# Performance work log

Measured on AMD Instinct MI355X. Metric: run time of the kernel, lower is better.

## Reference

```python
import jax, jax.numpy as jnp
import numpy as np

N = 100000      # nodes
E = 1600000     # edges (before self-loops)
IN = 128        # in_dim
HID = 128       # hidden_dim
H = 4           # heads
D = HID // H    # head_dim = 32
L = 3           # n_layers
G = 128         # graphs in batch
NEG_SLOPE = 0.2 # PyG GATConv default leaky_relu slope
BN_EPS = 1e-5


def setup_inputs() -> dict:
    key = jax.random.key(0)
    ks = jax.random.split(key, 16)
    x = jax.random.normal(ks[0], (N, IN), dtype=jnp.float32)
    edge_index = jax.random.randint(ks[1], (2, E), 0, N, dtype=jnp.int64)
    batch = jnp.sort(jax.random.randint(ks[2], (N,), 0, G, dtype=jnp.int64))
    # stacked per-layer GATConv params (in_dim == hidden_dim so all layers stack)
    W = jax.random.normal(ks[3], (L, HID, HID), dtype=jnp.float32) * (1.0 / np.sqrt(HID))
    att_src = jax.random.normal(ks[4], (L, H, D), dtype=jnp.float32) * 0.1
    att_dst = jax.random.normal(ks[5], (L, H, D), dtype=jnp.float32) * 0.1
    bias = jax.random.normal(ks[6], (L, HID), dtype=jnp.float32) * 0.01
    # BatchNorm1d (eval mode: running stats)
    gamma = 1.0 + 0.1 * jax.random.normal(ks[7], (L, HID), dtype=jnp.float32)
    beta = 0.01 * jax.random.normal(ks[8], (L, HID), dtype=jnp.float32)
    bn_mean = jnp.zeros((L, HID), dtype=jnp.float32)
    bn_var = jnp.ones((L, HID), dtype=jnp.float32)
    # MLP head: Linear(HID, HID//2) -> ReLU -> Linear(HID//2, 1)
    Wh1 = jax.random.normal(ks[9], (HID, HID // 2), dtype=jnp.float32) * (1.0 / np.sqrt(HID))
    bh1 = jnp.zeros((HID // 2,), dtype=jnp.float32)
    Wh2 = jax.random.normal(ks[10], (HID // 2, 1), dtype=jnp.float32) * (1.0 / np.sqrt(HID // 2))
    bh2 = jnp.zeros((1,), dtype=jnp.float32)
    return {"x": x, "edge_index": edge_index, "batch": batch, "W": W,
            "att_src": att_src, "att_dst": att_dst, "bias": bias,
            "gamma": gamma, "beta": beta, "bn_mean": bn_mean, "bn_var": bn_var,
            "Wh1": Wh1, "bh1": bh1, "Wh2": Wh2, "bh2": bh2}


def _gat_conv(x, src, dst, W_l, asrc, adst, b):
    # x: [N, F_in]; src/dst: [E+N] (self-loops included); returns [N, H*D]
    h = (x @ W_l).reshape(N, H, D)                      # [N,H,D]
    a_s = jnp.einsum('nhd,hd->nh', h, asrc)             # [N,H]
    a_d = jnp.einsum('nhd,hd->nh', h, adst)
    e = jax.nn.leaky_relu(a_s[src] + a_d[dst], NEG_SLOPE)  # [Etot,H]
    # segment softmax over incoming edges per destination node
    e_max = jax.ops.segment_max(e, dst, num_segments=N)    # [N,H]
    p = jnp.exp(e - e_max[dst])
    denom = jax.ops.segment_sum(p, dst, num_segments=N)    # [N,H]
    alpha = p / (denom[dst] + 1e-16)                        # [Etot,H]
    msg = h[src] * alpha[:, :, None]                        # [Etot,H,D]
    out = jax.ops.segment_sum(msg, dst, num_segments=N)     # [N,H,D]
    return out.reshape(N, H * D) + b


def reference(x, edge_index, batch, W, att_src, att_dst, bias,
              gamma, beta, bn_mean, bn_var, Wh1, bh1, Wh2, bh2):
    # add self-loops once (PyG GATConv default add_self_loops=True)
    loop = jnp.arange(N, dtype=edge_index.dtype)
    src = jnp.concatenate([edge_index[0], loop])
    dst = jnp.concatenate([edge_index[1], loop])
    for l in range(L):
        x = _gat_conv(x, src, dst, W[l], att_src[l], att_dst[l], bias[l])
        x = jnp.maximum(x, 0.0)
        # BatchNorm1d, eval mode (dropout is identity in eval)
        x = (x - bn_mean[l]) * (gamma[l] / jnp.sqrt(bn_var[l] + BN_EPS)) + beta[l]
    # global mean pool over graphs
    sums = jax.ops.segment_sum(x, batch, num_segments=G)            # [G,HID]
    cnts = jax.ops.segment_sum(jnp.ones((N,), x.dtype), batch, num_segments=G)
    pooled = sums / jnp.maximum(cnts, 1.0)[:, None]
    hdn = jnp.maximum(pooled @ Wh1 + bh1, 0.0)
    return (hdn @ Wh2 + bh2).squeeze(-1)                            # [G]
```

## Files before the change

kernel.cpp:

```cpp
#include <hip/hip_runtime.h>
#include <hip/hip_fp16.h>


typedef __bf16 bf16x8 __attribute__((ext_vector_type(8)));
typedef float  f32x4  __attribute__((ext_vector_type(4)));
typedef unsigned int u32x4 __attribute__((ext_vector_type(4)));

#define BCOLS 144
#define BSTRIDE (BCOLS * 128)

#define MAXBKT 800
#define BCAP   4096

__global__ __launch_bounds__(256)
void k_bucket(const int* __restrict__ ei, unsigned int* __restrict__ bkt,
              int* __restrict__ bcnt, int Ne, int Nn, int nbkt) {
    __shared__ int lcnt[MAXBKT];
    __shared__ int lbase[MAXBKT];
    int tid = threadIdx.x;
    for (int i = tid; i < nbkt; i += 256) lcnt[i] = 0;
    __syncthreads();
    int chunk0 = blockIdx.x * 8192;
    int nnz = Ne + Nn;
    for (int i = 0; i < 32; ++i) {
        int e = chunk0 + i * 256 + tid;
        if (e < nnz) {
            int d = (e < Ne) ? ei[Ne + e] : (e - Ne);
            atomicAdd(&lcnt[d >> 7], 1);
        }
    }
    __syncthreads();
    for (int b = tid; b < nbkt; b += 256) {
        int c = lcnt[b];
        lbase[b] = (c > 0) ? atomicAdd(&bcnt[b], c) : 0;
        lcnt[b] = 0;
    }
    __syncthreads();
    for (int i = 0; i < 32; ++i) {
        int e = chunk0 + i * 256 + tid;
        if (e < nnz) {
            int s, d;
            if (e < Ne) { s = ei[e]; d = ei[Ne + e]; }
            else        { s = e - Ne; d = e - Ne; }
            int b = d >> 7;
            int r = atomicAdd(&lcnt[b], 1);
            bkt[(long)b * BCAP + lbase[b] + r] = ((unsigned)s << 7) | (unsigned)(d & 127);
        }
    }
}

__global__ __launch_bounds__(256)
void k_bhist(const unsigned int* __restrict__ bkt, const int* __restrict__ bcnt,
             int* __restrict__ deg, int Nn) {
    __shared__ int h[128];
    int b = blockIdx.x;
    int tid = threadIdx.x;
    if (tid < 128) h[tid] = 0;
    __syncthreads();
    int cnt = bcnt[b];
    const unsigned int* bp = bkt + (long)b * BCAP;
    for (int i = tid; i < cnt; i += 256)
        atomicAdd(&h[bp[i] & 127], 1);
    __syncthreads();
    int node = b * 128 + tid;
    if (tid < 128 && node < Nn) deg[node] = h[tid];
}

__global__ __launch_bounds__(256)
void k_bscatter(const unsigned int* __restrict__ bkt, const int* __restrict__ bcnt,
                const int* __restrict__ rowptr, int* __restrict__ colv, int Nn) {
    __shared__ int cur[128];
    int b = blockIdx.x;
    int tid = threadIdx.x;
    int node = b * 128 + tid;
    if (tid < 128) cur[tid] = (node < Nn) ? rowptr[node] : 0;
    __syncthreads();
    int cnt = bcnt[b];
    const unsigned int* bp = bkt + (long)b * BCAP;
    for (int i = tid; i < cnt; i += 256) {
        unsigned int e = bp[i];
        int pos = atomicAdd(&cur[e & 127], 1);
        colv[pos] = (int)(e >> 7);
    }
}

__global__ __launch_bounds__(512)
void k_scan_partial(int* __restrict__ deg, int* __restrict__ tmp,
                    int* __restrict__ bsum, int Nn) {
    __shared__ int s0[512], s1[512];
    int t = threadIdx.x;
    int gi = blockIdx.x * 512 + t;
    int v = (gi < Nn) ? deg[gi] : 0;
    s0[t] = v;
    __syncthreads();
    int* src = s0; int* dst = s1;
    for (int off = 1; off < 512; off <<= 1) {
        int x = src[t];
        if (t >= off) x += src[t - off];
        dst[t] = x;
        __syncthreads();
        int* tw = src; src = dst; dst = tw;
    }
    if (gi < Nn) tmp[gi] = src[t];
    if (t == 511) bsum[blockIdx.x] = src[511];
}

__global__ __launch_bounds__(256)
void k_scan_bsums(int* bsum, int nb) {
    __shared__ int s0[256], s1[256];
    int t = threadIdx.x;
    int v = (t < nb) ? bsum[t] : 0;
    s0[t] = v;
    __syncthreads();
    int* src = s0; int* dst = s1;
    for (int off = 1; off < 256; off <<= 1) {
        int x = src[t];
        if (t >= off) x += src[t - off];
        dst[t] = x;
        __syncthreads();
        int* tw = src; src = dst; dst = tw;
    }
    if (t < nb) bsum[t] = src[t] - v;
}

__global__ void k_scan_add(const int* __restrict__ tmp, const int* __restrict__ bsum,
                           int* __restrict__ rowptr, int Nn) {
    int gi = blockIdx.x * 256 + threadIdx.x;
    if (gi < Nn) rowptr[gi + 1] = tmp[gi] + bsum[gi >> 9];
    if (gi == 0) rowptr[0] = 0;
}

__global__ void k_prep(const float* __restrict__ gamma, const float* __restrict__ beta,
                       const float* __restrict__ mean, const float* __restrict__ var,
                       float* __restrict__ bn_mul, float* __restrict__ bn_add,
                       const float* __restrict__ W, const float* __restrict__ asrc,
                       const float* __restrict__ adst,
                       __bf16* __restrict__ Hi, __bf16* __restrict__ Lo) {
    int gid = blockIdx.x * 256 + threadIdx.x;
    if (gid < 384) {
        float sc = gamma[gid] / sqrtf(var[gid] + 1e-5f);
        bn_mul[gid] = sc;
        bn_add[gid] = beta[gid] - mean[gid] * sc;
    }
    if (gid < 3 * 128 * 128) {
        int l = gid >> 14;
        int k = (gid >> 7) & 127;
        int n = gid & 127;
        float f = W[gid];
        __bf16 h = (__bf16)f;
        int o = l * BSTRIDE + n * 128 + k;
        Hi[o] = h;
        Lo[o] = (__bf16)(f - (float)h);
    }
    if (gid < 3 * 128 * 8) {
        int l = gid >> 10;
        int r = gid & 1023;
        int k = r >> 3;
        int j = r & 7;
        int hh = j & 3;
        const float* av = (j < 4 ? asrc : adst) + l * 128 + hh * 32;
        const float* wp = W + l * 16384 + k * 128 + hh * 32;
        float sum = 0.f;
#pragma unroll
        for (int d = 0; d < 32; ++d) sum = fmaf(wp[d], av[d], sum);
        __bf16 h = (__bf16)sum;
        int o = l * BSTRIDE + (128 + j) * 128 + k;
        Hi[o] = h;
        Lo[o] = (__bf16)(sum - (float)h);
    }
    if (gid < 3 * 128 * 8) {
        int l = gid >> 10;
        int r = gid & 1023;
        int k = r >> 3;
        int j = r & 7;
        int o = l * BSTRIDE + (136 + j) * 128 + k;
        Hi[o] = (__bf16)0.f;
        Lo[o] = (__bf16)0.f;
    }
}

__global__ __launch_bounds__(256)
void k_gemm_mfma(const float* __restrict__ X, const __bf16* __restrict__ BtHi,
                 const __bf16* __restrict__ BtLo, __half* __restrict__ Hout,
                 float* __restrict__ as_, float* __restrict__ ad_, int Nn) {
    int t = threadIdx.x;
    int w = t >> 6;
    int lane = t & 63;
    int li = lane & 15;
    int b  = lane >> 4;
    long rowBase = (long)blockIdx.x * 128 + w * 32;

    float4 xf[2][4][2];
#pragma unroll
    for (int rt = 0; rt < 2; ++rt) {
        long r = rowBase + rt * 16 + li;
        if (r > Nn - 1) r = Nn - 1;
        const float4* xp = (const float4*)(X + r * 128);
#pragma unroll
        for (int ks = 0; ks < 4; ++ks) {
            xf[rt][ks][0] = xp[ks * 8 + 2 * b];
            xf[rt][ks][1] = xp[ks * 8 + 2 * b + 1];
        }
    }

    f32x4 acc[2][9];
#pragma unroll
    for (int rt = 0; rt < 2; ++rt)
#pragma unroll
        for (int ct = 0; ct < 9; ++ct) acc[rt][ct] = (f32x4){0.f, 0.f, 0.f, 0.f};

#pragma unroll
    for (int ks = 0; ks < 4; ++ks) {
        int k0 = ks * 32 + 8 * b;
        bf16x8 ahi[2], alo[2];
#pragma unroll
        for (int rt = 0; rt < 2; ++rt) {
            float af[8] = {xf[rt][ks][0].x, xf[rt][ks][0].y, xf[rt][ks][0].z, xf[rt][ks][0].w,
                           xf[rt][ks][1].x, xf[rt][ks][1].y, xf[rt][ks][1].z, xf[rt][ks][1].w};
#pragma unroll
            for (int j = 0; j < 8; ++j) {
                __bf16 h = (__bf16)af[j];
                ahi[rt][j] = h;
                alo[rt][j] = (__bf16)(af[j] - (float)h);
            }
        }
#pragma unroll
        for (int ct = 0; ct < 9; ++ct) {
            int coff = (ct * 16 + li) * 128 + k0;
            bf16x8 bhi = *(const bf16x8*)(BtHi + coff);
            bf16x8 blo = *(const bf16x8*)(BtLo + coff);
#pragma unroll
            for (int rt = 0; rt < 2; ++rt) {
                acc[rt][ct] = __builtin_amdgcn_mfma_f32_16x16x32_bf16(ahi[rt], bhi, acc[rt][ct], 0, 0, 0);
                acc[rt][ct] = __builtin_amdgcn_mfma_f32_16x16x32_bf16(ahi[rt], blo, acc[rt][ct], 0, 0, 0);
                acc[rt][ct] = __builtin_amdgcn_mfma_f32_16x16x32_bf16(alo[rt], bhi, acc[rt][ct], 0, 0, 0);
            }
        }
    }

#pragma unroll
    for (int rt = 0; rt < 2; ++rt) {
#pragma unroll
        for (int reg = 0; reg < 4; ++reg) {
            long r = rowBase + rt * 16 + 4 * b + reg;
            if (r < Nn) {
                __half* op = Hout + r * 128 + li;
#pragma unroll
                for (int ct = 0; ct < 8; ++ct) op[ct * 16] = __float2half(acc[rt][ct][reg]);
                if (li < 4)      as_[4 * r + li]     = acc[rt][8][reg];
                else if (li < 8) ad_[4 * r + li - 4] = acc[rt][8][reg];
            }
        }
    }
}

#define LEAKY(x) ((x) > 0.f ? (x) : 0.2f * (x))

__global__ __launch_bounds__(256)
void k_aggregate(const __half* __restrict__ Hb, const float* __restrict__ as_,
                 const float* __restrict__ ad_, const int* __restrict__ rowptr,
                 const int* __restrict__ col, const float* __restrict__ bias,
                 const float* __restrict__ bn_mul, const float* __restrict__ bn_add,
                 float* __restrict__ Xout, int Nn) {
    __shared__ float s_alpha[4][64][4];
    __shared__ int   s_off[4][64];
    int w = threadIdx.x >> 6;
    int n = (blockIdx.x << 2) + w;
    if (n >= Nn) return;
    int lane = threadIdx.x & 63;
    int start = rowptr[n], end = rowptr[n + 1];
    int deg = end - start;

    if (deg <= 64) {
        int hh = lane & 3;
        int slot = lane >> 2;
        float adn = ad_[4 * n + hh];
        float esc[4]; int scl[4];
#pragma unroll
        for (int c = 0; c < 4; ++c) {
            int eidx = (c << 4) + slot;
            float e = -1e30f; int s = 0;
            if (eidx < deg) {
                s = col[start + eidx];
                e = LEAKY(as_[4 * s + hh] + adn);
            }
            esc[c] = e; scl[c] = s;
        }
        float m = fmaxf(fmaxf(esc[0], esc[1]), fmaxf(esc[2], esc[3]));
#pragma unroll
        for (int msk = 4; msk < 64; msk <<= 1) m = fmaxf(m, __shfl_xor(m, msk, 64));
        float p[4];
        float den = 0.f;
#pragma unroll
        for (int c = 0; c < 4; ++c) { p[c] = __expf(esc[c] - m); den += p[c]; }
#pragma unroll
        for (int msk = 4; msk < 64; msk <<= 1) den += __shfl_xor(den, msk, 64);
        float inv = 1.f / (den + 1e-16f);
#pragma unroll
        for (int c = 0; c < 4; ++c)
            s_alpha[w][(c << 4) + slot][hh] = p[c] * inv;
        if (hh == 0) {
#pragma unroll
            for (int c = 0; c < 4; ++c)
                s_off[w][(c << 4) + slot] = scl[c] << 8;
        }

        int quarter = lane >> 4;
        int li = lane & 15;
        int hB = li >> 2;
        int cByte = li << 4;
        const char* hb8 = (const char*)Hb;
        float accA[8], accB[8];
#pragma unroll
        for (int i = 0; i < 8; ++i) { accA[i] = 0.f; accB[i] = 0.f; }
        int degU = (deg + 7) & ~7;
        for (int j = 0; j < degU; j += 8) {
            int e0 = j + quarter;
            int e1 = j + 4 + quarter;
            int off0 = s_off[w][e0];
            int off1 = s_off[w][e1];
            float al0 = s_alpha[w][e0][hB];
            float al1 = s_alpha[w][e1][hB];
            u32x4 r0 = *(const u32x4*)(hb8 + off0 + cByte);
            u32x4 r1 = *(const u32x4*)(hb8 + off1 + cByte);
            const __half2* h0 = (const __half2*)&r0;
            const __half2* h1 = (const __half2*)&r1;
#pragma unroll
            for (int q = 0; q < 4; ++q) {
                float2 f0 = __half22float2(h0[q]);
                float2 f1 = __half22float2(h1[q]);
                accA[2 * q]     = fmaf(f0.x, al0, accA[2 * q]);
                accA[2 * q + 1] = fmaf(f0.y, al0, accA[2 * q + 1]);
                accB[2 * q]     = fmaf(f1.x, al1, accB[2 * q]);
                accB[2 * q + 1] = fmaf(f1.y, al1, accB[2 * q + 1]);
            }
        }
        float acc[8];
#pragma unroll
        for (int i = 0; i < 8; ++i) {
            float v = accA[i] + accB[i];
            v += __shfl_xor(v, 16, 64);
            v += __shfl_xor(v, 32, 64);
            acc[i] = v;
        }
        if (lane < 16) {
            int c0 = li << 3;
            float4 bz0 = *(const float4*)(bias + c0);
            float4 bz1 = *(const float4*)(bias + c0 + 4);
            float4 m0 = *(const float4*)(bn_mul + c0);
            float4 m1 = *(const float4*)(bn_mul + c0 + 4);
            float4 a0 = *(const float4*)(bn_add + c0);
            float4 a1 = *(const float4*)(bn_add + c0 + 4);
            float4 o0, o1;
            o0.x = fmaf(fmaxf(acc[0] + bz0.x, 0.f), m0.x, a0.x);
            o0.y = fmaf(fmaxf(acc[1] + bz0.y, 0.f), m0.y, a0.y);
            o0.z = fmaf(fmaxf(acc[2] + bz0.z, 0.f), m0.z, a0.z);
            o0.w = fmaf(fmaxf(acc[3] + bz0.w, 0.f), m0.w, a0.w);
            o1.x = fmaf(fmaxf(acc[4] + bz1.x, 0.f), m1.x, a1.x);
            o1.y = fmaf(fmaxf(acc[5] + bz1.y, 0.f), m1.y, a1.y);
            o1.z = fmaf(fmaxf(acc[6] + bz1.z, 0.f), m1.z, a1.z);
            o1.w = fmaf(fmaxf(acc[7] + bz1.w, 0.f), m1.w, a1.w);
            *(float4*)(Xout + (long)n * 128 + c0)     = o0;
            *(float4*)(Xout + (long)n * 128 + c0 + 4) = o1;
        }
        return;
    }

    int hh = lane & 3;
    float adn = ad_[n * 4 + hh];
    float m = -1e30f;
    for (int base = start; base < end; base += 16) {
        int idx = base + (lane >> 2);
        float sc = -1e30f;
        if (idx < end) {
            int s = col[idx];
            float e = as_[s * 4 + hh] + adn;
            sc = LEAKY(e);
        }
        m = fmaxf(m, sc);
    }
    for (int msk = 4; msk < 64; msk <<= 1) m = fmaxf(m, __shfl_xor(m, msk, 64));
    float den = 0.f;
    for (int base = start; base < end; base += 16) {
        int idx = base + (lane >> 2);
        if (idx < end) {
            int s = col[idx];
            float e = as_[s * 4 + hh] + adn;
            e = LEAKY(e);
            den += __expf(e - m);
        }
    }
    for (int msk = 4; msk < 64; msk <<= 1) den += __shfl_xor(den, msk, 64);
    int hB = lane >> 4;
    float mB   = __shfl(m, hB, 64);
    float invB = 1.f / (__shfl(den, hB, 64) + 1e-16f);
    float adB  = ad_[n * 4 + hB];
    int c0 = lane << 1;
    float acc0 = 0.f, acc1 = 0.f;
    for (int i = start; i < end; ++i) {
        int s = col[i];
        float e = as_[s * 4 + hB] + adB;
        e = LEAKY(e);
        float alpha = __expf(e - mB) * invB;
        float2 hv = __half22float2(*(const __half2*)(Hb + (long)s * 128 + c0));
        acc0 = fmaf(hv.x, alpha, acc0);
        acc1 = fmaf(hv.y, alpha, acc1);
    }
    float v0 = acc0 + bias[c0], v1 = acc1 + bias[c0 + 1];
    v0 = fmaxf(v0, 0.f); v1 = fmaxf(v1, 0.f);
    v0 = fmaf(v0, bn_mul[c0], bn_add[c0]);
    v1 = fmaf(v1, bn_mul[c0 + 1], bn_add[c0 + 1]);
    *(float2*)(Xout + (long)n * 128 + c0) = make_float2(v0, v1);
}

__global__ __launch_bounds__(128)
void k_pool(const float* __restrict__ X, const int* __restrict__ batch,
            float* __restrict__ gsum, int* __restrict__ gcnt, int Nn) {
    int c = threadIdx.x;
    int n0 = blockIdx.x * 64;
    if (n0 >= Nn) return;
    int nend = (n0 + 64 < Nn) ? n0 + 64 : Nn;
    float local = 0.f;
    int gcur = batch[n0];
    int cnt = 0;
    for (int n = n0; n < nend; ++n) {
        int g = batch[n];
        if (g != gcur) {
            atomicAdd(&gsum[gcur * 128 + c], local);
            if (c == 0) atomicAdd(&gcnt[gcur], cnt);
            local = 0.f; cnt = 0; gcur = g;
        }
        local += X[(long)n * 128 + c];
        cnt += 1;
    }
    atomicAdd(&gsum[gcur * 128 + c], local);
    if (c == 0) atomicAdd(&gcnt[gcur], cnt);
}

__global__ __launch_bounds__(64)
void k_head(const float* __restrict__ gsum, const int* __restrict__ gcnt,
            const float* __restrict__ Wh1, const float* __restrict__ bh1,
            const float* __restrict__ Wh2, const float* __restrict__ bh2,
            float* __restrict__ outp) {
    __shared__ float pooled[128];
    int g = blockIdx.x;
    int j = threadIdx.x;
    int cnt = gcnt[g];
    float inv = 1.f / (float)(cnt > 1 ? cnt : 1);
    pooled[j]      = gsum[g * 128 + j] * inv;
    pooled[j + 64] = gsum[g * 128 + 64 + j] * inv;
    __syncthreads();
    float acc = bh1[j];
    for (int k = 0; k < 128; ++k) acc = fmaf(pooled[k], Wh1[k * 64 + j], acc);
    acc = fmaxf(acc, 0.f);
    float prod = acc * Wh2[j];
    for (int msk = 1; msk < 64; msk <<= 1) prod += __shfl_xor(prod, msk, 64);
    if (j == 0) outp[g] = prod + bh2[0];
}

extern "C" void kernel_launch(void* const* d_in, const int* in_sizes, int n_in,
                              void* d_out, int out_size, void* d_ws, size_t ws_size,
                              hipStream_t stream) {
    const float* x       = (const float*)d_in[0];
    const int*   ei      = (const int*)d_in[1];
    const int*   batch   = (const int*)d_in[2];
    const float* W       = (const float*)d_in[3];
    const float* att_src = (const float*)d_in[4];
    const float* att_dst = (const float*)d_in[5];
    const float* bias    = (const float*)d_in[6];
    const float* gamma   = (const float*)d_in[7];
    const float* beta    = (const float*)d_in[8];
    const float* bn_mean = (const float*)d_in[9];
    const float* bn_var  = (const float*)d_in[10];
    const float* Wh1     = (const float*)d_in[11];
    const float* bh1     = (const float*)d_in[12];
    const float* Wh2     = (const float*)d_in[13];
    const float* bh2     = (const float*)d_in[14];
    float* out = (float*)d_out;

    const int Nn = in_sizes[0] / 128;
    const int Ne = in_sizes[1] / 2;
    const int Gg = out_size;
    const int nnz = Ne + Nn;
    const int nbkt = (Nn + 127) / 128;

    char* ws = (char*)d_ws;
    size_t off = 0;
    auto alloc = [&](size_t bytes) -> char* {
        char* p = ws + off;
        off = (off + bytes + 255) & ~(size_t)255;
        return p;
    };
    float*        bufA   = (float*)alloc((size_t)Nn * 128 * 4);
    __half*       bufH   = (__half*)alloc((size_t)Nn * 128 * 2);
    float*        as_    = (float*)alloc((size_t)Nn * 4 * 4);
    float*        ad_    = (float*)alloc((size_t)Nn * 4 * 4);
    int*          rowptr = (int*)alloc((size_t)(Nn + 1) * 4);
    int*          deg    = (int*)alloc((size_t)Nn * 4);
    int*          col    = (int*)alloc((size_t)nnz * 4);
    int*          bsum   = (int*)alloc(1024);
    float*        bn_mul = (float*)alloc(384 * 4);
    float*        bn_add = (float*)alloc(384 * 4);
    float*        gsum   = (float*)alloc((size_t)Gg * 128 * 4);
    int*          gcnt   = (int*)alloc((size_t)Gg * 4);
    __bf16*       WtHi   = (__bf16*)alloc((size_t)3 * BSTRIDE * 2);
    __bf16*       WtLo   = (__bf16*)alloc((size_t)3 * BSTRIDE * 2);
    unsigned int* bkt    = (unsigned int*)alloc((size_t)nbkt * BCAP * 4);
    int*          bcnt   = (int*)alloc((size_t)nbkt * 4);

    hipMemsetAsync(bcnt, 0, (size_t)nbkt * 4, stream);
    k_bucket<<<(nnz + 8191) / 8192, 256, 0, stream>>>(ei, bkt, bcnt, Ne, Nn, nbkt);
    k_bhist<<<nbkt, 256, 0, stream>>>(bkt, bcnt, deg, Nn);
    int nb = (Nn + 511) / 512;
    k_scan_partial<<<nb, 512, 0, stream>>>(deg, col, bsum, Nn);
    k_scan_bsums<<<1, 256, 0, stream>>>(bsum, nb);
    k_scan_add<<<(Nn + 255) / 256, 256, 0, stream>>>(col, bsum, rowptr, Nn);
    k_bscatter<<<nbkt, 256, 0, stream>>>(bkt, bcnt, rowptr, col, Nn);
    k_prep<<<192, 256, 0, stream>>>(gamma, beta, bn_mean, bn_var, bn_mul, bn_add,
                                    W, att_src, att_dst, WtHi, WtLo);

    const float* cur = x;
    for (int l = 0; l < 3; ++l) {
        k_gemm_mfma<<<(Nn + 127) / 128, 256, 0, stream>>>(cur, WtHi + l * BSTRIDE,
                                                          WtLo + l * BSTRIDE,
                                                          bufH, as_, ad_, Nn);
        k_aggregate<<<(Nn + 3) / 4, 256, 0, stream>>>(bufH, as_, ad_, rowptr, col,
                                                      bias + l * 128, bn_mul + l * 128,
                                                      bn_add + l * 128, bufA, Nn);
        cur = bufA;
    }

    hipMemsetAsync(gsum, 0, (size_t)Gg * 128 * 4, stream);
    hipMemsetAsync(gcnt, 0, (size_t)Gg * 4, stream);
    k_pool<<<(Nn + 63) / 64, 128, 0, stream>>>(bufA, batch, gsum, gcnt, Nn);
    k_head<<<Gg, 64, 0, stream>>>(gsum, gcnt, Wh1, bh1, Wh2, bh2, out);
}
```

Before: 578.7 us.

## Restructure CSR build: bucket-level scan, fused histogram+scatter, fewer launches

Replaces the per-node degree histogram plus three-pass node-level scan with a single-block scan over bucket counts, then computes per-node offsets inside the scatter kernel via a local 128-entry scan. The bucketing kernel now processes smaller chunks per block (2048 edges) for more parallelism and also zeroes the pooling accumulators, removing two memsets. This cuts kernel launches and global passes over degree arrays in the graph preprocessing phase, at the cost of more global atomics on bucket counters from the larger block count.

```diff
diff --git a/kernel.cpp b/kernel.cpp
--- a/kernel.cpp
+++ b/kernel.cpp
@@ -14,15 +14,19 @@
 
 __global__ __launch_bounds__(256)
 void k_bucket(const int* __restrict__ ei, unsigned int* __restrict__ bkt,
-              int* __restrict__ bcnt, int Ne, int Nn, int nbkt) {
+              int* __restrict__ bcnt, float* __restrict__ gsum,
+              int* __restrict__ gcnt, int Ne, int Nn, int nbkt, int Gg) {
     __shared__ int lcnt[MAXBKT];
     __shared__ int lbase[MAXBKT];
     int tid = threadIdx.x;
+    int gid = blockIdx.x * 256 + tid;
+    if (gid < Gg * 128) gsum[gid] = 0.f;
+    if (gid < Gg) gcnt[gid] = 0;
     for (int i = tid; i < nbkt; i += 256) lcnt[i] = 0;
     __syncthreads();
-    int chunk0 = blockIdx.x * 8192;
+    int chunk0 = blockIdx.x * 2048;
     int nnz = Ne + Nn;
-    for (int i = 0; i < 32; ++i) {
+    for (int i = 0; i < 8; ++i) {
         int e = chunk0 + i * 256 + tid;
         if (e < nnz) {
             int d = (e < Ne) ? ei[Ne + e] : (e - Ne);
@@ -36,7 +40,7 @@
         lcnt[b] = 0;
     }
     __syncthreads();
-    for (int i = 0; i < 32; ++i) {
+    for (int i = 0; i < 8; ++i) {
         int e = chunk0 + i * 256 + tid;
         if (e < nnz) {
             int s, d;
@@ -49,85 +53,64 @@
     }
 }
 
-__global__ __launch_bounds__(256)
-void k_bhist(const unsigned int* __restrict__ bkt, const int* __restrict__ bcnt,
-             int* __restrict__ deg, int Nn) {
-    __shared__ int h[128];
-    int b = blockIdx.x;
-    int tid = threadIdx.x;
-    if (tid < 128) h[tid] = 0;
-    __syncthreads();
-    int cnt = bcnt[b];
-    const unsigned int* bp = bkt + (long)b * BCAP;
-    for (int i = tid; i < cnt; i += 256)
-        atomicAdd(&h[bp[i] & 127], 1);
-    __syncthreads();
-    int node = b * 128 + tid;
-    if (tid < 128 && node < Nn) deg[node] = h[tid];
-}
-
-__global__ __launch_bounds__(256)
-void k_bscatter(const unsigned int* __restrict__ bkt, const int* __restrict__ bcnt,
-                const int* __restrict__ rowptr, int* __restrict__ colv, int Nn) {
-    __shared__ int cur[128];
-    int b = blockIdx.x;
-    int tid = threadIdx.x;
-    int node = b * 128 + tid;
-    if (tid < 128) cur[tid] = (node < Nn) ? rowptr[node] : 0;
-    __syncthreads();
-    int cnt = bcnt[b];
-    const unsigned int* bp = bkt + (long)b * BCAP;
-    for (int i = tid; i < cnt; i += 256) {
-        unsigned int e = bp[i];
-        int pos = atomicAdd(&cur[e & 127], 1);
-        colv[pos] = (int)(e >> 7);
-    }
-}
-
-__global__ __launch_bounds__(512)
-void k_scan_partial(int* __restrict__ deg, int* __restrict__ tmp,
-                    int* __restrict__ bsum, int Nn) {
-    __shared__ int s0[512], s1[512];
+__global__ __launch_bounds__(1024)
+void k_bktscan(const int* __restrict__ bcnt, int* __restrict__ bktbase, int nbkt) {
+    __shared__ int s0[1024], s1[1024];
     int t = threadIdx.x;
-    int gi = blockIdx.x * 512 + t;
-    int v = (gi < Nn) ? deg[gi] : 0;
+    int v = (t < nbkt) ? bcnt[t] : 0;
     s0[t] = v;
     __syncthreads();
     int* src = s0; int* dst = s1;
-    for (int off = 1; off < 512; off <<= 1) {
+    for (int off = 1; off < 1024; off <<= 1) {
         int x = src[t];
         if (t >= off) x += src[t - off];
         dst[t] = x;
         __syncthreads();
         int* tw = src; src = dst; dst = tw;
     }
-    if (gi < Nn) tmp[gi] = src[t];
-    if (t == 511) bsum[blockIdx.x] = src[511];
+    if (t < nbkt) bktbase[t] = src[t] - v;
 }
 
 __global__ __launch_bounds__(256)
-void k_scan_bsums(int* bsum, int nb) {
-    __shared__ int s0[256], s1[256];
-    int t = threadIdx.x;
-    int v = (t < nb) ? bsum[t] : 0;
-    s0[t] = v;
-    __syncthreads();
-    int* src = s0; int* dst = s1;
-    for (int off = 1; off < 256; off <<= 1) {
-        int x = src[t];
-        if (t >= off) x += src[t - off];
-        dst[t] = x;
+void k_bscatter2(const unsigned int* __restrict__ bkt, const int* __restrict__ bcnt,
+                 const int* __restrict__ bktbase, int* __restrict__ rowptr,
+                 int* __restrict__ colv, int Nn, int nnz) {
+    __shared__ int h[128], sc0[128], sc1[128];
+    int b = blockIdx.x;
+    int tid = threadIdx.x;
+    if (tid < 128) h[tid] = 0;
+    __syncthreads();
+    int cnt = bcnt[b];
+    int base = bktbase[b];
+    const unsigned int* bp = bkt + (long)b * BCAP;
+    for (int i = tid; i < cnt; i += 256) atomicAdd(&h[bp[i] & 127], 1);
+    __syncthreads();
+    if (tid < 128) sc0[tid] = h[tid];
+    __syncthreads();
+    int* src = sc0; int* dst = sc1;
+    for (int off = 1; off < 128; off <<= 1) {
+        if (tid < 128) {
+            int x = src[tid];
+            if (tid >= off) x += src[tid - off];
+            dst[tid] = x;
+        }
         __syncthreads();
         int* tw = src; src = dst; dst = tw;
     }
-    if (t < nb) bsum[t] = src[t] - v;
-}
-
-__global__ void k_scan_add(const int* __restrict__ tmp, const int* __restrict__ bsum,
-                           int* __restrict__ rowptr, int Nn) {
-    int gi = blockIdx.x * 256 + threadIdx.x;
-    if (gi < Nn) rowptr[gi + 1] = tmp[gi] + bsum[gi >> 9];
-    if (gi == 0) rowptr[0] = 0;
+    int node = b * 128 + tid;
+    if (tid < 128) {
+        int excl = src[tid] - h[tid];
+        int st = base + excl;
+        h[tid] = st;
+        if (node < Nn) rowptr[node] = st;
+    }
+    if (b == 0 && tid == 0) rowptr[Nn] = nnz;
+    __syncthreads();
+    for (int i = tid; i < cnt; i += 256) {
+        unsigned int e = bp[i];
+        int pos = atomicAdd(&h[e & 127], 1);
+        colv[pos] = (int)(e >> 7);
+    }
 }
 
 __global__ void k_prep(const float* __restrict__ gamma, const float* __restrict__ beta,
@@ -491,33 +474,29 @@
         off = (off + bytes + 255) & ~(size_t)255;
         return p;
     };
-    float*        bufA   = (float*)alloc((size_t)Nn * 128 * 4);
-    __half*       bufH   = (__half*)alloc((size_t)Nn * 128 * 2);
-    float*        as_    = (float*)alloc((size_t)Nn * 4 * 4);
-    float*        ad_    = (float*)alloc((size_t)Nn * 4 * 4);
-    int*          rowptr = (int*)alloc((size_t)(Nn + 1) * 4);
-    int*          deg    = (int*)alloc((size_t)Nn * 4);
-    int*          col    = (int*)alloc((size_t)nnz * 4);
-    int*          bsum   = (int*)alloc(1024);
-    float*        bn_mul = (float*)alloc(384 * 4);
-    float*        bn_add = (float*)alloc(384 * 4);
-    float*        gsum   = (float*)alloc((size_t)Gg * 128 * 4);
-    int*          gcnt   = (int*)alloc((size_t)Gg * 4);
-    __bf16*       WtHi   = (__bf16*)alloc((size_t)3 * BSTRIDE * 2);
-    __bf16*       WtLo   = (__bf16*)alloc((size_t)3 * BSTRIDE * 2);
-    unsigned int* bkt    = (unsigned int*)alloc((size_t)nbkt * BCAP * 4);
-    int*          bcnt   = (int*)alloc((size_t)nbkt * 4);
+    float*        bufA    = (float*)alloc((size_t)Nn * 128 * 4);
+    __half*       bufH    = (__half*)alloc((size_t)Nn * 128 * 2);
+    float*        as_     = (float*)alloc((size_t)Nn * 4 * 4);
+    float*        ad_     = (float*)alloc((size_t)Nn * 4 * 4);
+    int*          rowptr  = (int*)alloc((size_t)(Nn + 1) * 4);
+    int*          col     = (int*)alloc((size_t)nnz * 4);
+    float*        bn_mul  = (float*)alloc(384 * 4);
+    float*        bn_add  = (float*)alloc(384 * 4);
+    float*        gsum    = (float*)alloc((size_t)Gg * 128 * 4);
+    int*          gcnt    = (int*)alloc((size_t)Gg * 4);
+    __bf16*       WtHi    = (__bf16*)alloc((size_t)3 * BSTRIDE * 2);
+    __bf16*       WtLo    = (__bf16*)alloc((size_t)3 * BSTRIDE * 2);
+    unsigned int* bkt     = (unsigned int*)alloc((size_t)nbkt * BCAP * 4);
+    int*          bcnt    = (int*)alloc((size_t)nbkt * 4);
+    int*          bktbase = (int*)alloc((size_t)nbkt * 4);
 
     hipMemsetAsync(bcnt, 0, (size_t)nbkt * 4, stream);
-    k_bucket<<<(nnz + 8191) / 8192, 256, 0, stream>>>(ei, bkt, bcnt, Ne, Nn, nbkt);
-    k_bhist<<<nbkt, 256, 0, stream>>>(bkt, bcnt, deg, Nn);
-    int nb = (Nn + 511) / 512;
-    k_scan_partial<<<nb, 512, 0, stream>>>(deg, col, bsum, Nn);
-    k_scan_bsums<<<1, 256, 0, stream>>>(bsum, nb);
-    k_scan_add<<<(Nn + 255) / 256, 256, 0, stream>>>(col, bsum, rowptr, Nn);
-    k_bscatter<<<nbkt, 256, 0, stream>>>(bkt, bcnt, rowptr, col, Nn);
     k_prep<<<192, 256, 0, stream>>>(gamma, beta, bn_mean, bn_var, bn_mul, bn_add,
                                     W, att_src, att_dst, WtHi, WtLo);
+    k_bucket<<<(nnz + 2047) / 2048, 256, 0, stream>>>(ei, bkt, bcnt, gsum, gcnt,
+                                                      Ne, Nn, nbkt, Gg);
+    k_bktscan<<<1, 1024, 0, stream>>>(bcnt, bktbase, nbkt);
+    k_bscatter2<<<nbkt, 256, 0, stream>>>(bkt, bcnt, bktbase, rowptr, col, Nn, nnz);
 
     const float* cur = x;
     for (int l = 0; l < 3; ++l) {
@@ -530,8 +509,6 @@
         cur = bufA;
     }
 
-    hipMemsetAsync(gsum, 0, (size_t)Gg * 128 * 4, stream);
-    hipMemsetAsync(gcnt, 0, (size_t)Gg * 4, stream);
     k_pool<<<(Nn + 63) / 64, 128, 0, stream>>>(bufA, batch, gsum, gcnt, Nn);
     k_head<<<Gg, 64, 0, stream>>>(gsum, gcnt, Wh1, bh1, Wh2, bh2, out);
 }
```

Result: no change. 574.4 us (-0.7%).
